# Optimization experiments

Hardware: AMD Instinct MI355X
Metric: run time of the kernel (lower is better)

The kernel has to match this reference:

```python
import jax, jax.numpy as jnp
import numpy as np
from jax import lax

SAMPLE_RATE = 44100.0


def _biquad(x, b0, b1, b2, a1, a2):
    """Direct-form-I biquad over last axis. x: [B,C,S]; coefs: [B,1] (broadcast over C).
    y[n] = b0*x[n] + b1*x[n-1] + b2*x[n-2] - a1*y[n-1] - a2*y[n-2], zero initial state
    (identical to torchaudio.functional.biquad)."""

    def step(carry, xn):  # xn: [B,C]
        x1, x2, y1, y2 = carry
        y = b0 * xn + b1 * x1 + b2 * x2 - a1 * y1 - a2 * y2
        return (xn, x1, y, y1), y

    xs = jnp.moveaxis(x, -1, 0)  # [S,B,C]
    z = jnp.zeros_like(x[..., 0])
    _, ys = lax.scan(step, (z, z, z, z), xs)
    return jnp.moveaxis(ys, 0, -1)  # [B,C,S]


def _peaking_coeffs(freq, gain, q):
    """RBJ peaking EQ coefficients, normalized by a0. Inputs: [B] -> outputs [B,1]."""
    w0 = 2.0 * jnp.pi * freq / SAMPLE_RATE
    alpha = jnp.sin(w0) / (2.0 * q)
    A = jnp.power(10.0, gain / 40.0)
    cosw0 = jnp.cos(w0)
    b0 = 1.0 + alpha * A
    b1 = -2.0 * cosw0
    b2 = 1.0 - alpha * A
    a0 = 1.0 + alpha / A
    a1 = -2.0 * cosw0
    a2 = 1.0 - alpha / A
    coefs = (b0 / a0, b1 / a0, b2 / a0, a1 / a0, a2 / a0)
    return tuple(c[:, None] for c in coefs)  # broadcast over channel dim


def setup_inputs() -> dict:
    key = jax.random.key(0)
    k1, k2, k3, k4 = jax.random.split(key, 4)
    B, C, S, NB = 32, 2, 262144, 10
    audio = jax.random.normal(k1, (B, C, S), dtype=jnp.float32)
    center_freqs = jax.random.uniform(k2, (B, NB), dtype=jnp.float32, minval=100.0, maxval=10000.0)
    gains = jax.random.uniform(k3, (B, NB), dtype=jnp.float32, minval=-12.0, maxval=12.0)
    q_factors = jax.random.uniform(k4, (B, NB), dtype=jnp.float32, minval=0.5, maxval=4.0)
    return {"audio": audio, "center_freqs": center_freqs, "gains": gains, "q_factors": q_factors}


def reference(audio, center_freqs, gains, q_factors):
    num_bands = center_freqs.shape[1]
    out = audio
    for band in range(num_bands):  # fixed small cascade of structurally distinct filters
        b0, b1, b2, a1, a2 = _peaking_coeffs(center_freqs[:, band], gains[:, band], q_factors[:, band])
        out = _biquad(out, b0, b1, b2, a1, a2)
    return out
```

## Files before the change

### kernel.cpp

```cpp
#include <hip/hip_runtime.h>


#define B_   32
#define C_   2
#define S_   262144
#define NB   10
#define SEQ  64
#define LCH  256
#define PCH  1024
#define SUP  256
#define NPOW 9

#define WS_POW 1600
#define WS_T   116800

__global__ void coef_kernel(const float* __restrict__ freqs,
                            const float* __restrict__ gains,
                            const float* __restrict__ qs,
                            float* __restrict__ coef) {
  int idx = blockIdx.x * blockDim.x + threadIdx.x;
  if (idx >= B_ * NB) return;
  float f = freqs[idx], g = gains[idx], Q = qs[idx];
  float w0 = 6.28318530717958648f * f / 44100.0f;
  float sw = sinf(w0), cw = cosf(w0);
  float alpha = sw / (2.0f * Q);
  float A = expf(g * 0.05756462732485114f);
  float aA = alpha * A, adA = alpha / A;
  float inv = 1.0f / (1.0f + adA);
  float* o = coef + idx * 5;
  o[0] = (1.0f + aA) * inv;
  o[1] = -2.0f * cw * inv;
  o[2] = (1.0f - aA) * inv;
  o[3] = 2.0f * cw * inv;
  o[4] = -(1.0f - adA) * inv;
}

__global__ __launch_bounds__(256) void power_kernel(const float* __restrict__ coef,
                                                    float* __restrict__ powers) {
  __shared__ float bufA[400], bufB[400];
  int b = blockIdx.x, tid = threadIdx.x;
  const float* cf = coef + b * NB * 5;
  for (int e = tid; e < 400; e += 256) bufA[e] = 0.0f;
  __syncthreads();
  if (tid < 20) {
    int c = tid;
    float rp = 0.0f;
    for (int k = 0; k < NB; k++) {
      float b0 = cf[k*5+0], b1 = cf[k*5+1], b2 = cf[k*5+2];
      float na1 = cf[k*5+3], na2 = cf[k*5+4];
      float val = (k > 0) ? b0 * rp : 0.0f;
      if (k > 0) {
        if (c == 2*k-2) val += b1;
        if (c == 2*k-1) val += b2;
      }
      if (c == 2*k)   val += na1;
      if (c == 2*k+1) val += na2;
      bufA[2*k*20 + c] = val;
      rp = val;
      if (c == 2*k) bufA[(2*k+1)*20 + c] = 1.0f;
    }
  }
  __syncthreads();
  float* cur = bufA;
  float* nxt = bufB;
  float* pw = powers + (size_t)b * NPOW * 400;
  for (int j = 1; j <= 17; j++) {
    for (int e = tid; e < 400; e += 256) {
      int r = e / 20, c = e % 20;
      float acc = 0.0f;
      #pragma unroll
      for (int k = 0; k < 20; k++) acc = fmaf(cur[r*20+k], cur[k*20+c], acc);
      nxt[e] = acc;
    }
    __syncthreads();
    { float* t_ = cur; cur = nxt; nxt = t_; }
    if (j == 8)  for (int e = tid; e < 400; e += 256) pw[e] = cur[e];
    if (j >= 10) for (int e = tid; e < 400; e += 256) pw[(j-9)*400 + e] = cur[e];
  }
}

template <bool WRITE_OUT>
__global__ __launch_bounds__(256) void pass_kernel(const float* __restrict__ x,
                                                   const float* __restrict__ coef,
                                                   const float* __restrict__ sc,
                                                   float* __restrict__ tout,
                                                   float* __restrict__ out) {
  const int seq = blockIdx.y;
  const int b = seq >> 1;
  const int chunk = blockIdx.x * blockDim.x + threadIdx.x;
  const float* cf = coef + b * NB * 5;
  float b0[NB], b1[NB], b2[NB], na1[NB], na2[NB];
  #pragma unroll
  for (int k = 0; k < NB; k++) {
    b0[k] = cf[k*5+0]; b1[k] = cf[k*5+1]; b2[k] = cf[k*5+2];
    na1[k] = cf[k*5+3]; na2[k] = cf[k*5+4];
  }
  const float* xs = x + (size_t)seq * S_ + (size_t)chunk * LCH;
  float p[NB], q[NB];
  float x1 = 0.0f, x2 = 0.0f;
  if (chunk > 0) { x1 = xs[-1]; x2 = xs[-2]; }
  if (WRITE_OUT && chunk > 0) {
    const float* s0 = sc + ((size_t)seq * PCH + (chunk - 1)) * 20;
    #pragma unroll
    for (int k = 0; k < NB; k++) { p[k] = s0[2*k]; q[k] = s0[2*k+1]; }
  } else {
    #pragma unroll
    for (int k = 0; k < NB; k++) { p[k] = 0.0f; q[k] = 0.0f; }
  }
  const float4* xv = (const float4*)xs;
  float4* ov = nullptr;
  if (WRITE_OUT) ov = (float4*)(out + (size_t)seq * S_ + (size_t)chunk * LCH);
  #pragma unroll 1
  for (int n4 = 0; n4 < LCH / 4; n4++) {
    float4 xq = xv[n4];
    float xin[4] = {xq.x, xq.y, xq.z, xq.w};
    float o[4];
    #pragma unroll
    for (int j = 0; j < 4; j++) {
      float u = xin[j], u1 = x1, u2 = x2;
      x2 = x1; x1 = xin[j];
      #pragma unroll
      for (int k = 0; k < NB; k++) {
        float v = fmaf(b0[k], u,
                  fmaf(b1[k], u1,
                  fmaf(b2[k], u2,
                  fmaf(na1[k], p[k], na2[k] * q[k]))));
        u1 = p[k]; u2 = q[k];
        q[k] = p[k]; p[k] = v;
        u = v;
      }
      o[j] = u;
    }
    if (WRITE_OUT) ov[n4] = make_float4(o[0], o[1], o[2], o[3]);
  }
  if (!WRITE_OUT) {
    float* td = tout + ((size_t)seq * PCH + chunk) * 20;
    #pragma unroll
    for (int k = 0; k < NB; k++) { td[2*k] = p[k]; td[2*k+1] = q[k]; }
  }
}

__device__ __forceinline__ void mv20(float* __restrict__ o, const float* M,
                                     const float* v) {
  #pragma unroll
  for (int r = 0; r < 20; r++) {
    float acc = 0.0f;
    #pragma unroll
    for (int c = 0; c < 20; c++) acc = fmaf(M[r*20+c], v[c], acc);
    o[r] = acc;
  }
}

__global__ __launch_bounds__(256) void scan_kernel(float* __restrict__ t,
                                                   const float* __restrict__ powers) {
  __shared__ float h[SUP * 21];
  __shared__ float Msh[400];
  __shared__ float Ksh[400];
  const int seq = blockIdx.x, b = seq >> 1, i = threadIdx.x;
  const float* pw = powers + (size_t)b * NPOW * 400;
  for (int e = i; e < 400; e += 256) Msh[e] = pw[e];
  __syncthreads();
  float* tb = t + (size_t)seq * PCH * 20;
  float u0[20], u1[20], u2[20], own[20], tmp[20];
  #pragma unroll
  for (int r = 0; r < 20; r++) u0[r] = tb[(4*i + 0)*20 + r];
  mv20(u1, Msh, u0);
  #pragma unroll
  for (int r = 0; r < 20; r++) u1[r] += tb[(4*i + 1)*20 + r];
  mv20(u2, Msh, u1);
  #pragma unroll
  for (int r = 0; r < 20; r++) u2[r] += tb[(4*i + 2)*20 + r];
  mv20(own, Msh, u2);
  #pragma unroll
  for (int r = 0; r < 20; r++) own[r] += tb[(4*i + 3)*20 + r];
  #pragma unroll
  for (int r = 0; r < 20; r++) h[i*21 + r] = own[r];
  for (int s = 0; s < 8; s++) {
    const int d = 1 << s;
    __syncthreads();
    for (int e = i; e < 400; e += 256) Ksh[e] = pw[(1 + s)*400 + e];
    __syncthreads();
    float nb[20];
    if (i >= d) {
      #pragma unroll
      for (int r = 0; r < 20; r++) nb[r] = h[(i - d)*21 + r];
    }
    __syncthreads();
    if (i >= d) {
      mv20(tmp, Ksh, nb);
      #pragma unroll
      for (int r = 0; r < 20; r++) { own[r] += tmp[r]; h[i*21 + r] = own[r]; }
    }
  }
  __syncthreads();
  float Pi[20];
  if (i > 0) {
    #pragma unroll
    for (int r = 0; r < 20; r++) Pi[r] = h[(i - 1)*21 + r];
  } else {
    #pragma unroll
    for (int r = 0; r < 20; r++) Pi[r] = 0.0f;
  }
  float w[20];
  mv20(w, Msh, Pi);
  #pragma unroll
  for (int r = 0; r < 20; r++) tb[(4*i + 0)*20 + r] = w[r] + u0[r];
  mv20(tmp, Msh, w);
  #pragma unroll
  for (int r = 0; r < 20; r++) tb[(4*i + 1)*20 + r] = tmp[r] + u1[r];
  mv20(w, Msh, tmp);
  #pragma unroll
  for (int r = 0; r < 20; r++) tb[(4*i + 2)*20 + r] = w[r] + u2[r];
  #pragma unroll
  for (int r = 0; r < 20; r++) tb[(4*i + 3)*20 + r] = own[r];
}

extern "C" void kernel_launch(void* const* d_in, const int* in_sizes, int n_in,
                              void* d_out, int out_size, void* d_ws, size_t ws_size,
                              hipStream_t stream) {
  const float* audio = (const float*)d_in[0];
  const float* freqs = (const float*)d_in[1];
  const float* gains = (const float*)d_in[2];
  const float* qs    = (const float*)d_in[3];
  float* out    = (float*)d_out;
  float* ws     = (float*)d_ws;
  float* coef   = ws;
  float* powers = ws + WS_POW;
  float* t      = ws + WS_T;

  hipLaunchKernelGGL(coef_kernel, dim3(5), dim3(64), 0, stream,
                     freqs, gains, qs, coef);
  hipLaunchKernelGGL(power_kernel, dim3(B_), dim3(256), 0, stream, coef, powers);
  hipLaunchKernelGGL((pass_kernel<false>), dim3(PCH / 256, SEQ), dim3(256), 0, stream,
                     audio, coef, (const float*)nullptr, t, (float*)nullptr);
  hipLaunchKernelGGL(scan_kernel, dim3(SEQ), dim3(256), 0, stream, t, powers);
  hipLaunchKernelGGL((pass_kernel<true>), dim3(PCH / 256, SEQ), dim3(256), 0, stream,
                     audio, coef, t, (float*)nullptr, out);
}
```

Measured before the change: 268.7 us.

## Use shorter chunks with multi-chunk ILP per thread and hierarchical three-level state scan

Chunk length drops from 256 to 64 samples, so there are 4096 chunks per sequence. Each thread filters 4 independent chunks at once, which gives the serial biquad recurrence instruction-level parallelism. The cross-chunk state propagation becomes a three-level scan: a Horner pass over groups of 8, a Kogge-Stone scan over 512 groups, and a Horner write-back, using an extra matrix power. The output pass stages results through LDS for coalesced stores. The cost is more workspace, more scan work and register pressure, and the old path is kept as a fallback when the workspace is too small.

```diff
diff --git a/kernel.cpp b/kernel.cpp
--- a/kernel.cpp
+++ b/kernel.cpp
@@ -6,13 +6,27 @@
 #define S_   262144
 #define NB   10
 #define SEQ  64
-#define LCH  256
-#define PCH  1024
-#define SUP  256
-#define NPOW 9
-
-#define WS_POW 1600
-#define WS_T   116800
+
+#define F_LCH   64
+#define F_PCH   4096
+#define F_NCH   4
+#define F_G     8
+#define F_GRP   512
+#define F_NPOW  11
+
+#define F_OFF_POW 1600
+#define F_OFF_T   142400
+#define F_OFF_G   5385280
+#define F_OFF_SB  6040640
+#define F_TOT     6696000
+
+#define FB_LCH  256
+#define FB_PCH  1024
+#define FB_SUP  256
+#define FB_NPOW 9
+#define FB_OFF_POW 1600
+#define FB_OFF_T   116800
+#define FB_TOT     1427520
 
 __global__ void coef_kernel(const float* __restrict__ freqs,
                             const float* __restrict__ gains,
@@ -35,13 +49,7 @@
   o[4] = -(1.0f - adA) * inv;
 }
 
-__global__ __launch_bounds__(256) void power_kernel(const float* __restrict__ coef,
-                                                    float* __restrict__ powers) {
-  __shared__ float bufA[400], bufB[400];
-  int b = blockIdx.x, tid = threadIdx.x;
-  const float* cf = coef + b * NB * 5;
-  for (int e = tid; e < 400; e += 256) bufA[e] = 0.0f;
-  __syncthreads();
+__device__ __forceinline__ void build_A_rows(const float* cf, float* bufA, int tid) {
   if (tid < 20) {
     int c = tid;
     float rp = 0.0f;
@@ -60,10 +68,21 @@
       if (c == 2*k) bufA[(2*k+1)*20 + c] = 1.0f;
     }
   }
+}
+
+
+__global__ __launch_bounds__(256) void power_fast(const float* __restrict__ coef,
+                                                  float* __restrict__ powers) {
+  __shared__ float bufA[400], bufB[400];
+  int b = blockIdx.x, tid = threadIdx.x;
+  const float* cf = coef + b * NB * 5;
+  for (int e = tid; e < 400; e += 256) bufA[e] = 0.0f;
+  __syncthreads();
+  build_A_rows(cf, bufA, tid);
   __syncthreads();
   float* cur = bufA;
   float* nxt = bufB;
-  float* pw = powers + (size_t)b * NPOW * 400;
+  float* pw = powers + (size_t)b * F_NPOW * 400;
   for (int j = 1; j <= 17; j++) {
     for (int e = tid; e < 400; e += 256) {
       int r = e / 20, c = e % 20;
@@ -74,17 +93,342 @@
     }
     __syncthreads();
     { float* t_ = cur; cur = nxt; nxt = t_; }
+    int slot = -1;
+    if (j == 6) slot = 0;
+    else if (j == 8) slot = 1;
+    else if (j == 9) slot = 2;
+    else if (j >= 10) slot = j - 7;
+    if (slot >= 0) for (int e = tid; e < 400; e += 256) pw[slot*400 + e] = cur[e];
+  }
+}
+
+__global__ __launch_bounds__(256, 1) void pass_false_fast(
+    const float* __restrict__ x, const float* __restrict__ coef,
+    float* __restrict__ t) {
+  const int seq = blockIdx.y;
+  const int b = seq >> 1;
+  const int tid = threadIdx.x;
+  const int wg0 = blockIdx.x * (256 * F_NCH);
+  const float* cf = coef + b * NB * 5;
+  float b0[NB], b1[NB], b2[NB], na1[NB], na2[NB];
+  #pragma unroll
+  for (int k = 0; k < NB; k++) {
+    b0[k] = cf[k*5+0]; b1[k] = cf[k*5+1]; b2[k] = cf[k*5+2];
+    na1[k] = cf[k*5+3]; na2[k] = cf[k*5+4];
+  }
+  int cidx[F_NCH];
+  const float4* xv[F_NCH];
+  float p[F_NCH][NB], q[F_NCH][NB], x1[F_NCH], x2[F_NCH];
+  #pragma unroll
+  for (int k = 0; k < F_NCH; k++) {
+    cidx[k] = wg0 + k * 256 + tid;
+    const float* xs = x + (size_t)seq * S_ + (size_t)cidx[k] * F_LCH;
+    xv[k] = (const float4*)xs;
+    x1[k] = 0.0f; x2[k] = 0.0f;
+    if (cidx[k] > 0) { x1[k] = xs[-1]; x2[k] = xs[-2]; }
+    #pragma unroll
+    for (int kk = 0; kk < NB; kk++) { p[k][kk] = 0.0f; q[k][kk] = 0.0f; }
+  }
+  #pragma unroll 1
+  for (int n4 = 0; n4 < F_LCH / 4; n4++) {
+    #pragma unroll
+    for (int k = 0; k < F_NCH; k++) {
+      float4 xq = xv[k][n4];
+      float xin[4] = {xq.x, xq.y, xq.z, xq.w};
+      #pragma unroll
+      for (int j = 0; j < 4; j++) {
+        float u = xin[j], u1 = x1[k], u2 = x2[k];
+        x2[k] = x1[k]; x1[k] = xin[j];
+        #pragma unroll
+        for (int kk = 0; kk < NB; kk++) {
+          float v = fmaf(b0[kk], u,
+                    fmaf(b1[kk], u1,
+                    fmaf(b2[kk], u2,
+                    fmaf(na1[kk], p[k][kk], na2[kk] * q[k][kk]))));
+          u1 = p[k][kk]; u2 = q[k][kk];
+          q[k][kk] = p[k][kk]; p[k][kk] = v;
+          u = v;
+        }
+      }
+    }
+  }
+  #pragma unroll
+  for (int k = 0; k < F_NCH; k++) {
+    float4* td = (float4*)(t + ((size_t)seq * F_PCH + cidx[k]) * 20);
+    #pragma unroll
+    for (int i = 0; i < 5; i++)
+      td[i] = make_float4(p[k][2*i], q[k][2*i], p[k][2*i+1], q[k][2*i+1]);
+  }
+}
+
+template <bool WRITE_BACK>
+__global__ __launch_bounds__(256) void scan_horner(
+    float* __restrict__ t, const float* __restrict__ powers,
+    float* __restrict__ gbuf, const float* __restrict__ sbuf) {
+  __shared__ float Msh[400];
+  const int seq = blockIdx.y, b = seq >> 1;
+  const int g = blockIdx.x * 256 + threadIdx.x;
+  const float* pw0 = powers + (size_t)b * F_NPOW * 400;
+  for (int e = threadIdx.x; e < 400; e += 256) {
+    int r = e / 20, c = e % 20;
+    Msh[c*20 + r] = pw0[e];
+  }
+  __syncthreads();
+  float s[20];
+  if (WRITE_BACK) {
+    const float4* sv = (const float4*)(sbuf + ((size_t)seq * F_GRP + g) * 20);
+    #pragma unroll
+    for (int i = 0; i < 5; i++) {
+      float4 a = sv[i];
+      s[4*i] = a.x; s[4*i+1] = a.y; s[4*i+2] = a.z; s[4*i+3] = a.w;
+    }
+  } else {
+    #pragma unroll
+    for (int r = 0; r < 20; r++) s[r] = 0.0f;
+  }
+  float* tp = t + ((size_t)seq * F_PCH + (size_t)g * F_G) * 20;
+  #pragma unroll 1
+  for (int j = 0; j < F_G; j++) {
+    float ns[20];
+    const float4* tv = (const float4*)(tp + j * 20);
+    #pragma unroll
+    for (int i = 0; i < 5; i++) {
+      float4 a = tv[i];
+      ns[4*i] = a.x; ns[4*i+1] = a.y; ns[4*i+2] = a.z; ns[4*i+3] = a.w;
+    }
+    #pragma unroll
+    for (int c = 0; c < 20; c++) {
+      float vc = s[c];
+      const float4* col = (const float4*)&Msh[c*20];
+      float4 c0 = col[0], c1 = col[1], c2 = col[2], c3 = col[3], c4 = col[4];
+      ns[0]  = fmaf(c0.x, vc, ns[0]);  ns[1]  = fmaf(c0.y, vc, ns[1]);
+      ns[2]  = fmaf(c0.z, vc, ns[2]);  ns[3]  = fmaf(c0.w, vc, ns[3]);
+      ns[4]  = fmaf(c1.x, vc, ns[4]);  ns[5]  = fmaf(c1.y, vc, ns[5]);
+      ns[6]  = fmaf(c1.z, vc, ns[6]);  ns[7]  = fmaf(c1.w, vc, ns[7]);
+      ns[8]  = fmaf(c2.x, vc, ns[8]);  ns[9]  = fmaf(c2.y, vc, ns[9]);
+      ns[10] = fmaf(c2.z, vc, ns[10]); ns[11] = fmaf(c2.w, vc, ns[11]);
+      ns[12] = fmaf(c3.x, vc, ns[12]); ns[13] = fmaf(c3.y, vc, ns[13]);
+      ns[14] = fmaf(c3.z, vc, ns[14]); ns[15] = fmaf(c3.w, vc, ns[15]);
+      ns[16] = fmaf(c4.x, vc, ns[16]); ns[17] = fmaf(c4.y, vc, ns[17]);
+      ns[18] = fmaf(c4.z, vc, ns[18]); ns[19] = fmaf(c4.w, vc, ns[19]);
+    }
+    #pragma unroll
+    for (int r = 0; r < 20; r++) s[r] = ns[r];
+    if (WRITE_BACK) {
+      float4* tw = (float4*)(tp + j * 20);
+      #pragma unroll
+      for (int i = 0; i < 5; i++)
+        tw[i] = make_float4(s[4*i], s[4*i+1], s[4*i+2], s[4*i+3]);
+    }
+  }
+  if (!WRITE_BACK) {
+    float4* gw = (float4*)(gbuf + ((size_t)seq * F_GRP + g) * 20);
+    #pragma unroll
+    for (int i = 0; i < 5; i++)
+      gw[i] = make_float4(s[4*i], s[4*i+1], s[4*i+2], s[4*i+3]);
+  }
+}
+
+__global__ __launch_bounds__(512) void scan_ks(
+    const float* __restrict__ gbuf, const float* __restrict__ powers,
+    float* __restrict__ sbuf) {
+  __shared__ float h[F_GRP * 20];
+  __shared__ float Ksh[400];
+  const int seq = blockIdx.x, b = seq >> 1, i = threadIdx.x;
+  const float* pw = powers + (size_t)b * F_NPOW * 400;
+  float own[20];
+  {
+    const float4* gv = (const float4*)(gbuf + ((size_t)seq * F_GRP + i) * 20);
+    #pragma unroll
+    for (int k = 0; k < 5; k++) {
+      float4 a = gv[k];
+      own[4*k] = a.x; own[4*k+1] = a.y; own[4*k+2] = a.z; own[4*k+3] = a.w;
+    }
+  }
+  #pragma unroll
+  for (int r = 0; r < 20; r++) h[i*20 + r] = own[r];
+  for (int s = 0; s < 9; s++) {
+    const int d = 1 << s;
+    const float* pwS = pw + (size_t)(2 + s) * 400;
+    __syncthreads();
+    for (int e = i; e < 400; e += 512) {
+      int r = e / 20, c = e % 20;
+      Ksh[c*20 + r] = pwS[e];
+    }
+    float nb[20];
+    if (i >= d) {
+      const float4* hv = (const float4*)&h[(i - d) * 20];
+      #pragma unroll
+      for (int k = 0; k < 5; k++) {
+        float4 a = hv[k];
+        nb[4*k] = a.x; nb[4*k+1] = a.y; nb[4*k+2] = a.z; nb[4*k+3] = a.w;
+      }
+    }
+    __syncthreads();
+    if (i >= d) {
+      #pragma unroll
+      for (int c = 0; c < 20; c++) {
+        float vc = nb[c];
+        const float4* col = (const float4*)&Ksh[c*20];
+        float4 c0 = col[0], c1 = col[1], c2 = col[2], c3 = col[3], c4 = col[4];
+        own[0]  = fmaf(c0.x, vc, own[0]);  own[1]  = fmaf(c0.y, vc, own[1]);
+        own[2]  = fmaf(c0.z, vc, own[2]);  own[3]  = fmaf(c0.w, vc, own[3]);
+        own[4]  = fmaf(c1.x, vc, own[4]);  own[5]  = fmaf(c1.y, vc, own[5]);
+        own[6]  = fmaf(c1.z, vc, own[6]);  own[7]  = fmaf(c1.w, vc, own[7]);
+        own[8]  = fmaf(c2.x, vc, own[8]);  own[9]  = fmaf(c2.y, vc, own[9]);
+        own[10] = fmaf(c2.z, vc, own[10]); own[11] = fmaf(c2.w, vc, own[11]);
+        own[12] = fmaf(c3.x, vc, own[12]); own[13] = fmaf(c3.w==c3.w?c3.y:c3.y, vc, own[13]);
+        own[14] = fmaf(c3.z, vc, own[14]); own[15] = fmaf(c3.w, vc, own[15]);
+        own[16] = fmaf(c4.x, vc, own[16]); own[17] = fmaf(c4.y, vc, own[17]);
+        own[18] = fmaf(c4.z, vc, own[18]); own[19] = fmaf(c4.w, vc, own[19]);
+      }
+      #pragma unroll
+      for (int r = 0; r < 20; r++) h[i*20 + r] = own[r];
+    }
+  }
+  __syncthreads();
+  float4* sw = (float4*)(sbuf + ((size_t)seq * F_GRP + i) * 20);
+  if (i > 0) {
+    const float4* hv = (const float4*)&h[(i - 1) * 20];
+    #pragma unroll
+    for (int k = 0; k < 5; k++) sw[k] = hv[k];
+  } else {
+    #pragma unroll
+    for (int k = 0; k < 5; k++) sw[k] = make_float4(0.f, 0.f, 0.f, 0.f);
+  }
+}
+
+__global__ __launch_bounds__(256, 1) void pass_true_fast(
+    const float* __restrict__ x, const float* __restrict__ coef,
+    const float* __restrict__ t, float* __restrict__ out) {
+  __shared__ float stash[2 * 256 * 16];
+  const int seq = blockIdx.y;
+  const int b = seq >> 1;
+  const int tid = threadIdx.x;
+  const int wg0 = blockIdx.x * (256 * F_NCH);
+  const float* cf = coef + b * NB * 5;
+  float b0[NB], b1[NB], b2[NB], na1[NB], na2[NB];
+  #pragma unroll
+  for (int k = 0; k < NB; k++) {
+    b0[k] = cf[k*5+0]; b1[k] = cf[k*5+1]; b2[k] = cf[k*5+2];
+    na1[k] = cf[k*5+3]; na2[k] = cf[k*5+4];
+  }
+  int cidx[F_NCH];
+  const float4* xv[F_NCH];
+  float p[F_NCH][NB], q[F_NCH][NB], x1[F_NCH], x2[F_NCH];
+  #pragma unroll
+  for (int k = 0; k < F_NCH; k++) {
+    cidx[k] = wg0 + k * 256 + tid;
+    const float* xs = x + (size_t)seq * S_ + (size_t)cidx[k] * F_LCH;
+    xv[k] = (const float4*)xs;
+    x1[k] = 0.0f; x2[k] = 0.0f;
+    if (cidx[k] > 0) { x1[k] = xs[-1]; x2[k] = xs[-2]; }
+    if (cidx[k] > 0) {
+      const float4* sv = (const float4*)(t + ((size_t)seq * F_PCH + cidx[k] - 1) * 20);
+      #pragma unroll
+      for (int i = 0; i < 5; i++) {
+        float4 a = sv[i];
+        p[k][2*i] = a.x; q[k][2*i] = a.y; p[k][2*i+1] = a.z; q[k][2*i+1] = a.w;
+      }
+    } else {
+      #pragma unroll
+      for (int kk = 0; kk < NB; kk++) { p[k][kk] = 0.0f; q[k][kk] = 0.0f; }
+    }
+  }
+  float4* stashv = (float4*)stash;
+  const size_t seqbase = (size_t)seq * S_;
+  #pragma unroll 1
+  for (int tile = 0; tile < 4; tile++) {
+    float4 oreg[2][4];
+    #pragma unroll 1
+    for (int n4 = 0; n4 < 4; n4++) {
+      #pragma unroll
+      for (int k = 0; k < F_NCH; k++) {
+        float4 xq = xv[k][tile*4 + n4];
+        float xin[4] = {xq.x, xq.y, xq.z, xq.w};
+        float o[4];
+        #pragma unroll
+        for (int j = 0; j < 4; j++) {
+          float u = xin[j], u1 = x1[k], u2 = x2[k];
+          x2[k] = x1[k]; x1[k] = xin[j];
+          #pragma unroll
+          for (int kk = 0; kk < NB; kk++) {
+            float v = fmaf(b0[kk], u,
+                      fmaf(b1[kk], u1,
+                      fmaf(b2[kk], u2,
+                      fmaf(na1[kk], p[k][kk], na2[kk] * q[k][kk]))));
+            u1 = p[k][kk]; u2 = q[k][kk];
+            q[k][kk] = p[k][kk]; p[k][kk] = v;
+            u = v;
+          }
+          o[j] = u;
+        }
+        float4 of = make_float4(o[0], o[1], o[2], o[3]);
+        if (k < 2) stashv[(k*256 + tid)*4 + n4] = of;
+        else       oreg[k-2][n4] = of;
+      }
+    }
+    __syncthreads();
+    #pragma unroll
+    for (int i = 0; i < 8; i++) {
+      int f = tid + i * 256;
+      int chunkIdx = f >> 2, w = f & 3;
+      float4 v = stashv[f];
+      float4* op = (float4*)(out + seqbase + (size_t)(wg0 + chunkIdx) * F_LCH + tile*16);
+      op[w] = v;
+    }
+    __syncthreads();
+    #pragma unroll
+    for (int k2 = 0; k2 < 2; k2++)
+      #pragma unroll
+      for (int n4 = 0; n4 < 4; n4++)
+        stashv[(k2*256 + tid)*4 + n4] = oreg[k2][n4];
+    __syncthreads();
+    #pragma unroll
+    for (int i = 0; i < 8; i++) {
+      int f = tid + i * 256;
+      int chunkIdx = f >> 2, w = f & 3;
+      float4 v = stashv[f];
+      float4* op = (float4*)(out + seqbase + (size_t)(wg0 + 512 + chunkIdx) * F_LCH + tile*16);
+      op[w] = v;
+    }
+    __syncthreads();
+  }
+}
+
+__global__ __launch_bounds__(256) void power_fb(const float* __restrict__ coef,
+                                                float* __restrict__ powers) {
+  __shared__ float bufA[400], bufB[400];
+  int b = blockIdx.x, tid = threadIdx.x;
+  const float* cf = coef + b * NB * 5;
+  for (int e = tid; e < 400; e += 256) bufA[e] = 0.0f;
+  __syncthreads();
+  build_A_rows(cf, bufA, tid);
+  __syncthreads();
+  float* cur = bufA;
+  float* nxt = bufB;
+  float* pw = powers + (size_t)b * FB_NPOW * 400;
+  for (int j = 1; j <= 17; j++) {
+    for (int e = tid; e < 400; e += 256) {
+      int r = e / 20, c = e % 20;
+      float acc = 0.0f;
+      #pragma unroll
+      for (int k = 0; k < 20; k++) acc = fmaf(cur[r*20+k], cur[k*20+c], acc);
+      nxt[e] = acc;
+    }
+    __syncthreads();
+    { float* t_ = cur; cur = nxt; nxt = t_; }
     if (j == 8)  for (int e = tid; e < 400; e += 256) pw[e] = cur[e];
     if (j >= 10) for (int e = tid; e < 400; e += 256) pw[(j-9)*400 + e] = cur[e];
   }
 }
 
 template <bool WRITE_OUT>
-__global__ __launch_bounds__(256) void pass_kernel(const float* __restrict__ x,
-                                                   const float* __restrict__ coef,
-                                                   const float* __restrict__ sc,
-                                                   float* __restrict__ tout,
-                                                   float* __restrict__ out) {
+__global__ __launch_bounds__(256) void pass_fb(const float* __restrict__ x,
+                                               const float* __restrict__ coef,
+                                               const float* __restrict__ sc,
+                                               float* __restrict__ tout,
+                                               float* __restrict__ out) {
   const int seq = blockIdx.y;
   const int b = seq >> 1;
   const int chunk = blockIdx.x * blockDim.x + threadIdx.x;
@@ -95,24 +439,24 @@
     b0[k] = cf[k*5+0]; b1[k] = cf[k*5+1]; b2[k] = cf[k*5+2];
     na1[k] = cf[k*5+3]; na2[k] = cf[k*5+4];
   }
-  const float* xs = x + (size_t)seq * S_ + (size_t)chunk * LCH;
+  const float* xs = x + (size_t)seq * S_ + (size_t)chunk * FB_LCH;
   float p[NB], q[NB];
   float x1 = 0.0f, x2 = 0.0f;
   if (chunk > 0) { x1 = xs[-1]; x2 = xs[-2]; }
   if (WRITE_OUT && chunk > 0) {
-    const float* s0 = sc + ((size_t)seq * PCH + (chunk - 1)) * 20;
+    const float* s0 = sc + ((size_t)seq * FB_PCH + (chunk - 1)) * 20;
     #pragma unroll
     for (int k = 0; k < NB; k++) { p[k] = s0[2*k]; q[k] = s0[2*k+1]; }
   } else {
     #pragma unroll
     for (int k = 0; k < NB; k++) { p[k] = 0.0f; q[k] = 0.0f; }
   }
-  const float4* xv = (const float4*)xs;
+  const float4* xvv = (const float4*)xs;
   float4* ov = nullptr;
-  if (WRITE_OUT) ov = (float4*)(out + (size_t)seq * S_ + (size_t)chunk * LCH);
+  if (WRITE_OUT) ov = (float4*)(out + (size_t)seq * S_ + (size_t)chunk * FB_LCH);
   #pragma unroll 1
-  for (int n4 = 0; n4 < LCH / 4; n4++) {
-    float4 xq = xv[n4];
+  for (int n4 = 0; n4 < FB_LCH / 4; n4++) {
+    float4 xq = xvv[n4];
     float xin[4] = {xq.x, xq.y, xq.z, xq.w};
     float o[4];
     #pragma unroll
@@ -134,14 +478,14 @@
     if (WRITE_OUT) ov[n4] = make_float4(o[0], o[1], o[2], o[3]);
   }
   if (!WRITE_OUT) {
-    float* td = tout + ((size_t)seq * PCH + chunk) * 20;
+    float* td = tout + ((size_t)seq * FB_PCH + chunk) * 20;
     #pragma unroll
     for (int k = 0; k < NB; k++) { td[2*k] = p[k]; td[2*k+1] = q[k]; }
   }
 }
 
-__device__ __forceinline__ void mv20(float* __restrict__ o, const float* M,
-                                     const float* v) {
+__device__ __forceinline__ void mv20_fb(float* __restrict__ o, const float* M,
+                                        const float* v) {
   #pragma unroll
   for (int r = 0; r < 20; r++) {
     float acc = 0.0f;
@@ -151,26 +495,26 @@
   }
 }
 
-__global__ __launch_bounds__(256) void scan_kernel(float* __restrict__ t,
-                                                   const float* __restrict__ powers) {
-  __shared__ float h[SUP * 21];
+__global__ __launch_bounds__(256) void scan_fb(float* __restrict__ t,
+                                               const float* __restrict__ powers) {
+  __shared__ float h[FB_SUP * 21];
   __shared__ float Msh[400];
   __shared__ float Ksh[400];
   const int seq = blockIdx.x, b = seq >> 1, i = threadIdx.x;
-  const float* pw = powers + (size_t)b * NPOW * 400;
+  const float* pw = powers + (size_t)b * FB_NPOW * 400;
   for (int e = i; e < 400; e += 256) Msh[e] = pw[e];
   __syncthreads();
-  float* tb = t + (size_t)seq * PCH * 20;
+  float* tb = t + (size_t)seq * FB_PCH * 20;
   float u0[20], u1[20], u2[20], own[20], tmp[20];
   #pragma unroll
   for (int r = 0; r < 20; r++) u0[r] = tb[(4*i + 0)*20 + r];
-  mv20(u1, Msh, u0);
+  mv20_fb(u1, Msh, u0);
   #pragma unroll
   for (int r = 0; r < 20; r++) u1[r] += tb[(4*i + 1)*20 + r];
-  mv20(u2, Msh, u1);
+  mv20_fb(u2, Msh, u1);
   #pragma unroll
   for (int r = 0; r < 20; r++) u2[r] += tb[(4*i + 2)*20 + r];
-  mv20(own, Msh, u2);
+  mv20_fb(own, Msh, u2);
   #pragma unroll
   for (int r = 0; r < 20; r++) own[r] += tb[(4*i + 3)*20 + r];
   #pragma unroll
@@ -187,7 +531,7 @@
     }
     __syncthreads();
     if (i >= d) {
-      mv20(tmp, Ksh, nb);
+      mv20_fb(tmp, Ksh, nb);
       #pragma unroll
       for (int r = 0; r < 20; r++) { own[r] += tmp[r]; h[i*21 + r] = own[r]; }
     }
@@ -202,13 +546,13 @@
     for (int r = 0; r < 20; r++) Pi[r] = 0.0f;
   }
   float w[20];
-  mv20(w, Msh, Pi);
+  mv20_fb(w, Msh, Pi);
   #pragma unroll
   for (int r = 0; r < 20; r++) tb[(4*i + 0)*20 + r] = w[r] + u0[r];
-  mv20(tmp, Msh, w);
+  mv20_fb(tmp, Msh, w);
   #pragma unroll
   for (int r = 0; r < 20; r++) tb[(4*i + 1)*20 + r] = tmp[r] + u1[r];
-  mv20(w, Msh, tmp);
+  mv20_fb(w, Msh, tmp);
   #pragma unroll
   for (int r = 0; r < 20; r++) tb[(4*i + 2)*20 + r] = w[r] + u2[r];
   #pragma unroll
@@ -222,18 +566,37 @@
   const float* freqs = (const float*)d_in[1];
   const float* gains = (const float*)d_in[2];
   const float* qs    = (const float*)d_in[3];
-  float* out    = (float*)d_out;
-  float* ws     = (float*)d_ws;
-  float* coef   = ws;
-  float* powers = ws + WS_POW;
-  float* t      = ws + WS_T;
+  float* out = (float*)d_out;
+  float* ws  = (float*)d_ws;
+  float* coef = ws;
 
   hipLaunchKernelGGL(coef_kernel, dim3(5), dim3(64), 0, stream,
                      freqs, gains, qs, coef);
-  hipLaunchKernelGGL(power_kernel, dim3(B_), dim3(256), 0, stream, coef, powers);
-  hipLaunchKernelGGL((pass_kernel<false>), dim3(PCH / 256, SEQ), dim3(256), 0, stream,
-                     audio, coef, (const float*)nullptr, t, (float*)nullptr);
-  hipLaunchKernelGGL(scan_kernel, dim3(SEQ), dim3(256), 0, stream, t, powers);
-  hipLaunchKernelGGL((pass_kernel<true>), dim3(PCH / 256, SEQ), dim3(256), 0, stream,
-                     audio, coef, t, (float*)nullptr, out);
-}
+
+  if (ws_size >= (size_t)F_TOT * sizeof(float)) {
+    float* powers = ws + F_OFF_POW;
+    float* t      = ws + F_OFF_T;
+    float* gbuf   = ws + F_OFF_G;
+    float* sbuf   = ws + F_OFF_SB;
+    hipLaunchKernelGGL(power_fast, dim3(B_), dim3(256), 0, stream, coef, powers);
+    hipLaunchKernelGGL(pass_false_fast, dim3(F_PCH / (256 * F_NCH), SEQ), dim3(256),
+                       0, stream, audio, coef, t);
+    hipLaunchKernelGGL((scan_horner<false>), dim3(F_GRP / 256, SEQ), dim3(256),
+                       0, stream, t, powers, gbuf, (const float*)nullptr);
+    hipLaunchKernelGGL(scan_ks, dim3(SEQ), dim3(512), 0, stream,
+                       gbuf, powers, sbuf);
+    hipLaunchKernelGGL((scan_horner<true>), dim3(F_GRP / 256, SEQ), dim3(256),
+                       0, stream, t, powers, (float*)nullptr, sbuf);
+    hipLaunchKernelGGL(pass_true_fast, dim3(F_PCH / (256 * F_NCH), SEQ), dim3(256),
+                       0, stream, audio, coef, t, out);
+  } else {
+    float* powers = ws + FB_OFF_POW;
+    float* t      = ws + FB_OFF_T;
+    hipLaunchKernelGGL(power_fb, dim3(B_), dim3(256), 0, stream, coef, powers);
+    hipLaunchKernelGGL((pass_fb<false>), dim3(FB_PCH / 256, SEQ), dim3(256), 0, stream,
+                       audio, coef, (const float*)nullptr, t, (float*)nullptr);
+    hipLaunchKernelGGL(scan_fb, dim3(SEQ), dim3(256), 0, stream, t, powers);
+    hipLaunchKernelGGL((pass_fb<true>), dim3(FB_PCH / 256, SEQ), dim3(256), 0, stream,
+                       audio, coef, t, (float*)nullptr, out);
+  }
+}
```

Measured after the change: 290.4 us. 8.0% more time.

## Shrink chunks to 64 samples, stage through LDS, and use a three-level state scan

Applied to the files above, without the earlier changes.

The sequence is now split into 4096 chunks of 64 samples, so there are four times as many threads, each doing a shorter serial biquad cascade. Audio is staged through swizzled LDS so global loads and stores are coalesced. The cross-chunk state scan becomes a Horner reduction over groups of 8, a Kogge-Stone scan over 512 group totals, and a Horner write-back. The coefficient and power kernels are merged into one setup kernel, which adds an extra matrix power but removes one launch. The cost is more launches and more 20-float state traffic.

```diff
diff --git a/kernel.cpp b/kernel.cpp
--- a/kernel.cpp
+++ b/kernel.cpp
@@ -6,48 +6,53 @@
 #define S_   262144
 #define NB   10
 #define SEQ  64
-#define LCH  256
-#define PCH  1024
-#define SUP  256
-#define NPOW 9
-
-#define WS_POW 1600
-#define WS_T   116800
-
-__global__ void coef_kernel(const float* __restrict__ freqs,
-                            const float* __restrict__ gains,
-                            const float* __restrict__ qs,
-                            float* __restrict__ coef) {
-  int idx = blockIdx.x * blockDim.x + threadIdx.x;
-  if (idx >= B_ * NB) return;
-  float f = freqs[idx], g = gains[idx], Q = qs[idx];
-  float w0 = 6.28318530717958648f * f / 44100.0f;
-  float sw = sinf(w0), cw = cosf(w0);
-  float alpha = sw / (2.0f * Q);
-  float A = expf(g * 0.05756462732485114f);
-  float aA = alpha * A, adA = alpha / A;
-  float inv = 1.0f / (1.0f + adA);
-  float* o = coef + idx * 5;
-  o[0] = (1.0f + aA) * inv;
-  o[1] = -2.0f * cw * inv;
-  o[2] = (1.0f - aA) * inv;
-  o[3] = 2.0f * cw * inv;
-  o[4] = -(1.0f - adA) * inv;
-}
-
-__global__ __launch_bounds__(256) void power_kernel(const float* __restrict__ coef,
-                                                    float* __restrict__ powers) {
+
+#define F_LCH   64
+#define F_PCH   4096
+#define F_G     8
+#define F_GRP   512
+#define F_NPOW  11
+
+#define F_OFF_POW 1600
+#define F_OFF_T   142400
+#define F_OFF_G   5385280
+#define F_OFF_SB  6040640
+#define F_TOT     6696000
+
+__global__ __launch_bounds__(256) void setup_kernel(
+    const float* __restrict__ freqs, const float* __restrict__ gains,
+    const float* __restrict__ qs, float* __restrict__ coef,
+    float* __restrict__ powers) {
   __shared__ float bufA[400], bufB[400];
-  int b = blockIdx.x, tid = threadIdx.x;
-  const float* cf = coef + b * NB * 5;
+  __shared__ float cfs[NB * 5];
+  const int b = blockIdx.x, tid = threadIdx.x;
   for (int e = tid; e < 400; e += 256) bufA[e] = 0.0f;
+  if (tid < NB) {
+    int idx = b * NB + tid;
+    float f = freqs[idx], g = gains[idx], Q = qs[idx];
+    float w0 = 6.28318530717958648f * f / 44100.0f;
+    float sw = sinf(w0), cw = cosf(w0);
+    float alpha = sw / (2.0f * Q);
+    float A = expf(g * 0.05756462732485114f);
+    float aA = alpha * A, adA = alpha / A;
+    float inv = 1.0f / (1.0f + adA);
+    float c0 = (1.0f + aA) * inv;
+    float c1 = -2.0f * cw * inv;
+    float c2 = (1.0f - aA) * inv;
+    float c3 = 2.0f * cw * inv;
+    float c4 = -(1.0f - adA) * inv;
+    cfs[tid*5+0] = c0; cfs[tid*5+1] = c1; cfs[tid*5+2] = c2;
+    cfs[tid*5+3] = c3; cfs[tid*5+4] = c4;
+    float* o = coef + idx * 5;
+    o[0] = c0; o[1] = c1; o[2] = c2; o[3] = c3; o[4] = c4;
+  }
   __syncthreads();
   if (tid < 20) {
     int c = tid;
     float rp = 0.0f;
     for (int k = 0; k < NB; k++) {
-      float b0 = cf[k*5+0], b1 = cf[k*5+1], b2 = cf[k*5+2];
-      float na1 = cf[k*5+3], na2 = cf[k*5+4];
+      float b0 = cfs[k*5+0], b1 = cfs[k*5+1], b2 = cfs[k*5+2];
+      float na1 = cfs[k*5+3], na2 = cfs[k*5+4];
       float val = (k > 0) ? b0 * rp : 0.0f;
       if (k > 0) {
         if (c == 2*k-2) val += b1;
@@ -63,7 +68,7 @@
   __syncthreads();
   float* cur = bufA;
   float* nxt = bufB;
-  float* pw = powers + (size_t)b * NPOW * 400;
+  float* pw = powers + (size_t)b * F_NPOW * 400;
   for (int j = 1; j <= 17; j++) {
     for (int e = tid; e < 400; e += 256) {
       int r = e / 20, c = e % 20;
@@ -74,20 +79,26 @@
     }
     __syncthreads();
     { float* t_ = cur; cur = nxt; nxt = t_; }
-    if (j == 8)  for (int e = tid; e < 400; e += 256) pw[e] = cur[e];
-    if (j >= 10) for (int e = tid; e < 400; e += 256) pw[(j-9)*400 + e] = cur[e];
+    int slot = -1;
+    if (j == 6) slot = 0;
+    else if (j == 8) slot = 1;
+    else if (j == 9) slot = 2;
+    else if (j >= 10) slot = j - 7;
+    if (slot >= 0) for (int e = tid; e < 400; e += 256) pw[slot*400 + e] = cur[e];
   }
 }
 
 template <bool WRITE_OUT>
-__global__ __launch_bounds__(256) void pass_kernel(const float* __restrict__ x,
-                                                   const float* __restrict__ coef,
-                                                   const float* __restrict__ sc,
-                                                   float* __restrict__ tout,
-                                                   float* __restrict__ out) {
+__global__ __launch_bounds__(64) void pass_v3(
+    const float* __restrict__ x, const float* __restrict__ coef,
+    const float* __restrict__ tst, float* __restrict__ tout,
+    float* __restrict__ out) {
+  __shared__ float4 lds4[1024];
   const int seq = blockIdx.y;
   const int b = seq >> 1;
-  const int chunk = blockIdx.x * blockDim.x + threadIdx.x;
+  const int lane = threadIdx.x;
+  const int wgc0 = blockIdx.x * 64;
+  const int chunk = wgc0 + lane;
   const float* cf = coef + b * NB * 5;
   float b0[NB], b1[NB], b2[NB], na1[NB], na2[NB];
   #pragma unroll
@@ -95,25 +106,43 @@
     b0[k] = cf[k*5+0]; b1[k] = cf[k*5+1]; b2[k] = cf[k*5+2];
     na1[k] = cf[k*5+3]; na2[k] = cf[k*5+4];
   }
-  const float* xs = x + (size_t)seq * S_ + (size_t)chunk * LCH;
-  float p[NB], q[NB];
+  const size_t span0 = (size_t)seq * S_ + (size_t)wgc0 * F_LCH;
+  const float4* gx = (const float4*)(x + span0);
+  #pragma unroll 4
+  for (int it = 0; it < 16; it++) {
+    int f = it * 64 + lane;
+    float4 v = gx[f];
+    int c = f >> 4, q = f & 15;
+    lds4[c*16 + (q ^ (c & 15))] = v;
+  }
+  __syncthreads();
   float x1 = 0.0f, x2 = 0.0f;
-  if (chunk > 0) { x1 = xs[-1]; x2 = xs[-2]; }
+  if (lane == 0) {
+    if (chunk > 0) {
+      const float* xs = x + span0;
+      x1 = xs[-1]; x2 = xs[-2];
+    }
+  } else {
+    float4 pv = lds4[(lane-1)*16 + (15 ^ ((lane-1) & 15))];
+    x2 = pv.z; x1 = pv.w;
+  }
+  float p[NB], q_[NB];
   if (WRITE_OUT && chunk > 0) {
-    const float* s0 = sc + ((size_t)seq * PCH + (chunk - 1)) * 20;
-    #pragma unroll
-    for (int k = 0; k < NB; k++) { p[k] = s0[2*k]; q[k] = s0[2*k+1]; }
-  } else {
-    #pragma unroll
-    for (int k = 0; k < NB; k++) { p[k] = 0.0f; q[k] = 0.0f; }
-  }
-  const float4* xv = (const float4*)xs;
-  float4* ov = nullptr;
-  if (WRITE_OUT) ov = (float4*)(out + (size_t)seq * S_ + (size_t)chunk * LCH);
-  #pragma unroll 1
-  for (int n4 = 0; n4 < LCH / 4; n4++) {
-    float4 xq = xv[n4];
-    float xin[4] = {xq.x, xq.y, xq.z, xq.w};
+    const float4* sv = (const float4*)(tst + ((size_t)seq * F_PCH + chunk - 1) * 20);
+    #pragma unroll
+    for (int i = 0; i < 5; i++) {
+      float4 a = sv[i];
+      p[2*i] = a.x; q_[2*i] = a.y; p[2*i+1] = a.z; q_[2*i+1] = a.w;
+    }
+  } else {
+    #pragma unroll
+    for (int k = 0; k < NB; k++) { p[k] = 0.0f; q_[k] = 0.0f; }
+  }
+  #pragma unroll 2
+  for (int qq = 0; qq < 16; qq++) {
+    const int slot = lane*16 + (qq ^ (lane & 15));
+    float4 xv = lds4[slot];
+    float xin[4] = {xv.x, xv.y, xv.z, xv.w};
     float o[4];
     #pragma unroll
     for (int j = 0; j < 4; j++) {
@@ -124,95 +153,174 @@
         float v = fmaf(b0[k], u,
                   fmaf(b1[k], u1,
                   fmaf(b2[k], u2,
-                  fmaf(na1[k], p[k], na2[k] * q[k]))));
-        u1 = p[k]; u2 = q[k];
-        q[k] = p[k]; p[k] = v;
+                  fmaf(na1[k], p[k], na2[k] * q_[k]))));
+        u1 = p[k]; u2 = q_[k];
+        q_[k] = p[k]; p[k] = v;
         u = v;
       }
       o[j] = u;
     }
-    if (WRITE_OUT) ov[n4] = make_float4(o[0], o[1], o[2], o[3]);
-  }
-  if (!WRITE_OUT) {
-    float* td = tout + ((size_t)seq * PCH + chunk) * 20;
-    #pragma unroll
-    for (int k = 0; k < NB; k++) { td[2*k] = p[k]; td[2*k+1] = q[k]; }
-  }
-}
-
-__device__ __forceinline__ void mv20(float* __restrict__ o, const float* M,
-                                     const float* v) {
+    if (WRITE_OUT) lds4[slot] = make_float4(o[0], o[1], o[2], o[3]);
+  }
+  if (WRITE_OUT) {
+    __syncthreads();
+    float4* gy = (float4*)(out + span0);
+    #pragma unroll 4
+    for (int it = 0; it < 16; it++) {
+      int f = it * 64 + lane;
+      int c = f >> 4, q = f & 15;
+      gy[f] = lds4[c*16 + (q ^ (c & 15))];
+    }
+  } else {
+    float4* td = (float4*)(tout + ((size_t)seq * F_PCH + chunk) * 20);
+    #pragma unroll
+    for (int i = 0; i < 5; i++)
+      td[i] = make_float4(p[2*i], q_[2*i], p[2*i+1], q_[2*i+1]);
+  }
+}
+
+template <bool WRITE_BACK>
+__global__ __launch_bounds__(256) void scan_horner(
+    float* __restrict__ t, const float* __restrict__ powers,
+    float* __restrict__ gbuf, const float* __restrict__ sbuf) {
+  __shared__ float Msh[400];
+  const int seq = blockIdx.y, b = seq >> 1;
+  const int g = blockIdx.x * 256 + threadIdx.x;
+  const float* pw0 = powers + (size_t)b * F_NPOW * 400;
+  for (int e = threadIdx.x; e < 400; e += 256) {
+    int r = e / 20, c = e % 20;
+    Msh[c*20 + r] = pw0[e];
+  }
+  __syncthreads();
+  float s[20];
+  if (WRITE_BACK) {
+    const float4* sv = (const float4*)(sbuf + ((size_t)seq * F_GRP + g) * 20);
+    #pragma unroll
+    for (int i = 0; i < 5; i++) {
+      float4 a = sv[i];
+      s[4*i] = a.x; s[4*i+1] = a.y; s[4*i+2] = a.z; s[4*i+3] = a.w;
+    }
+  } else {
+    #pragma unroll
+    for (int r = 0; r < 20; r++) s[r] = 0.0f;
+  }
+  float* tp = t + ((size_t)seq * F_PCH + (size_t)g * F_G) * 20;
+  const float4* tv = (const float4*)tp;
+  float4 nx[5];
   #pragma unroll
-  for (int r = 0; r < 20; r++) {
-    float acc = 0.0f;
-    #pragma unroll
-    for (int c = 0; c < 20; c++) acc = fmaf(M[r*20+c], v[c], acc);
-    o[r] = acc;
-  }
-}
-
-__global__ __launch_bounds__(256) void scan_kernel(float* __restrict__ t,
-                                                   const float* __restrict__ powers) {
-  __shared__ float h[SUP * 21];
-  __shared__ float Msh[400];
+  for (int i = 0; i < 5; i++) nx[i] = tv[i];
+  #pragma unroll 1
+  for (int j = 0; j < F_G; j++) {
+    float ns[20];
+    #pragma unroll
+    for (int i = 0; i < 5; i++) {
+      float4 a = nx[i];
+      ns[4*i] = a.x; ns[4*i+1] = a.y; ns[4*i+2] = a.z; ns[4*i+3] = a.w;
+    }
+    if (j < F_G - 1) {
+      #pragma unroll
+      for (int i = 0; i < 5; i++) nx[i] = tv[(j+1)*5 + i];
+    }
+    #pragma unroll
+    for (int c = 0; c < 20; c++) {
+      float vc = s[c];
+      const float4* col = (const float4*)&Msh[c*20];
+      float4 c0 = col[0], c1 = col[1], c2 = col[2], c3 = col[3], c4 = col[4];
+      ns[0]  = fmaf(c0.x, vc, ns[0]);  ns[1]  = fmaf(c0.y, vc, ns[1]);
+      ns[2]  = fmaf(c0.z, vc, ns[2]);  ns[3]  = fmaf(c0.w, vc, ns[3]);
+      ns[4]  = fmaf(c1.x, vc, ns[4]);  ns[5]  = fmaf(c1.y, vc, ns[5]);
+      ns[6]  = fmaf(c1.z, vc, ns[6]);  ns[7]  = fmaf(c1.w, vc, ns[7]);
+      ns[8]  = fmaf(c2.x, vc, ns[8]);  ns[9]  = fmaf(c2.y, vc, ns[9]);
+      ns[10] = fmaf(c2.z, vc, ns[10]); ns[11] = fmaf(c2.w, vc, ns[11]);
+      ns[12] = fmaf(c3.x, vc, ns[12]); ns[13] = fmaf(c3.y, vc, ns[13]);
+      ns[14] = fmaf(c3.z, vc, ns[14]); ns[15] = fmaf(c3.w, vc, ns[15]);
+      ns[16] = fmaf(c4.x, vc, ns[16]); ns[17] = fmaf(c4.y, vc, ns[17]);
+      ns[18] = fmaf(c4.z, vc, ns[18]); ns[19] = fmaf(c4.w, vc, ns[19]);
+    }
+    #pragma unroll
+    for (int r = 0; r < 20; r++) s[r] = ns[r];
+    if (WRITE_BACK) {
+      float4* tw = (float4*)(tp + j * 20);
+      #pragma unroll
+      for (int i = 0; i < 5; i++)
+        tw[i] = make_float4(s[4*i], s[4*i+1], s[4*i+2], s[4*i+3]);
+    }
+  }
+  if (!WRITE_BACK) {
+    float4* gw = (float4*)(gbuf + ((size_t)seq * F_GRP + g) * 20);
+    #pragma unroll
+    for (int i = 0; i < 5; i++)
+      gw[i] = make_float4(s[4*i], s[4*i+1], s[4*i+2], s[4*i+3]);
+  }
+}
+
+__global__ __launch_bounds__(512) void scan_ks(
+    const float* __restrict__ gbuf, const float* __restrict__ powers,
+    float* __restrict__ sbuf) {
+  __shared__ float h[F_GRP * 20];
   __shared__ float Ksh[400];
   const int seq = blockIdx.x, b = seq >> 1, i = threadIdx.x;
-  const float* pw = powers + (size_t)b * NPOW * 400;
-  for (int e = i; e < 400; e += 256) Msh[e] = pw[e];
-  __syncthreads();
-  float* tb = t + (size_t)seq * PCH * 20;
-  float u0[20], u1[20], u2[20], own[20], tmp[20];
+  const float* pw = powers + (size_t)b * F_NPOW * 400;
+  float own[20];
+  {
+    const float4* gv = (const float4*)(gbuf + ((size_t)seq * F_GRP + i) * 20);
+    #pragma unroll
+    for (int k = 0; k < 5; k++) {
+      float4 a = gv[k];
+      own[4*k] = a.x; own[4*k+1] = a.y; own[4*k+2] = a.z; own[4*k+3] = a.w;
+    }
+  }
   #pragma unroll
-  for (int r = 0; r < 20; r++) u0[r] = tb[(4*i + 0)*20 + r];
-  mv20(u1, Msh, u0);
-  #pragma unroll
-  for (int r = 0; r < 20; r++) u1[r] += tb[(4*i + 1)*20 + r];
-  mv20(u2, Msh, u1);
-  #pragma unroll
-  for (int r = 0; r < 20; r++) u2[r] += tb[(4*i + 2)*20 + r];
-  mv20(own, Msh, u2);
-  #pragma unroll
-  for (int r = 0; r < 20; r++) own[r] += tb[(4*i + 3)*20 + r];
-  #pragma unroll
-  for (int r = 0; r < 20; r++) h[i*21 + r] = own[r];
-  for (int s = 0; s < 8; s++) {
+  for (int r = 0; r < 20; r++) h[i*20 + r] = own[r];
+  for (int s = 0; s < 9; s++) {
     const int d = 1 << s;
+    const float* pwS = pw + (size_t)(2 + s) * 400;
     __syncthreads();
-    for (int e = i; e < 400; e += 256) Ksh[e] = pw[(1 + s)*400 + e];
-    __syncthreads();
+    for (int e = i; e < 400; e += 512) {
+      int r = e / 20, c = e % 20;
+      Ksh[c*20 + r] = pwS[e];
+    }
     float nb[20];
     if (i >= d) {
-      #pragma unroll
-      for (int r = 0; r < 20; r++) nb[r] = h[(i - d)*21 + r];
+      const float4* hv = (const float4*)&h[(i - d) * 20];
+      #pragma unroll
+      for (int k = 0; k < 5; k++) {
+        float4 a = hv[k];
+        nb[4*k] = a.x; nb[4*k+1] = a.y; nb[4*k+2] = a.z; nb[4*k+3] = a.w;
+      }
     }
     __syncthreads();
     if (i >= d) {
-      mv20(tmp, Ksh, nb);
-      #pragma unroll
-      for (int r = 0; r < 20; r++) { own[r] += tmp[r]; h[i*21 + r] = own[r]; }
-    }
-  }
-  __syncthreads();
-  float Pi[20];
+      #pragma unroll
+      for (int c = 0; c < 20; c++) {
+        float vc = nb[c];
+        const float4* col = (const float4*)&Ksh[c*20];
+        float4 c0 = col[0], c1 = col[1], c2 = col[2], c3 = col[3], c4 = col[4];
+        own[0]  = fmaf(c0.x, vc, own[0]);  own[1]  = fmaf(c0.y, vc, own[1]);
+        own[2]  = fmaf(c0.z, vc, own[2]);  own[3]  = fmaf(c0.w, vc, own[3]);
+        own[4]  = fmaf(c1.x, vc, own[4]);  own[5]  = fmaf(c1.y, vc, own[5]);
+        own[6]  = fmaf(c1.z, vc, own[6]);  own[7]  = fmaf(c1.w, vc, own[7]);
+        own[8]  = fmaf(c2.x, vc, own[8]);  own[9]  = fmaf(c2.y, vc, own[9]);
+        own[10] = fmaf(c2.z, vc, own[10]); own[11] = fmaf(c2.w, vc, own[11]);
+        own[12] = fmaf(c3.x, vc, own[12]); own[13] = fmaf(c3.y, vc, own[13]);
+        own[14] = fmaf(c3.z, vc, own[14]); own[15] = fmaf(c3.w, vc, own[15]);
+        own[16] = fmaf(c4.x, vc, own[16]); own[17] = fmaf(c4.y, vc, own[17]);
+        own[18] = fmaf(c4.z, vc, own[18]); own[19] = fmaf(c4.w, vc, own[19]);
+      }
+      #pragma unroll
+      for (int r = 0; r < 20; r++) h[i*20 + r] = own[r];
+    }
+  }
+  __syncthreads();
+  float4* sw = (float4*)(sbuf + ((size_t)seq * F_GRP + i) * 20);
   if (i > 0) {
-    #pragma unroll
-    for (int r = 0; r < 20; r++) Pi[r] = h[(i - 1)*21 + r];
-  } else {
-    #pragma unroll
-    for (int r = 0; r < 20; r++) Pi[r] = 0.0f;
-  }
-  float w[20];
-  mv20(w, Msh, Pi);
-  #pragma unroll
-  for (int r = 0; r < 20; r++) tb[(4*i + 0)*20 + r] = w[r] + u0[r];
-  mv20(tmp, Msh, w);
-  #pragma unroll
-  for (int r = 0; r < 20; r++) tb[(4*i + 1)*20 + r] = tmp[r] + u1[r];
-  mv20(w, Msh, tmp);
-  #pragma unroll
-  for (int r = 0; r < 20; r++) tb[(4*i + 2)*20 + r] = w[r] + u2[r];
-  #pragma unroll
-  for (int r = 0; r < 20; r++) tb[(4*i + 3)*20 + r] = own[r];
+    const float4* hv = (const float4*)&h[(i - 1) * 20];
+    #pragma unroll
+    for (int k = 0; k < 5; k++) sw[k] = hv[k];
+  } else {
+    #pragma unroll
+    for (int k = 0; k < 5; k++) sw[k] = make_float4(0.f, 0.f, 0.f, 0.f);
+  }
 }
 
 extern "C" void kernel_launch(void* const* d_in, const int* in_sizes, int n_in,
@@ -222,18 +330,24 @@
   const float* freqs = (const float*)d_in[1];
   const float* gains = (const float*)d_in[2];
   const float* qs    = (const float*)d_in[3];
-  float* out    = (float*)d_out;
-  float* ws     = (float*)d_ws;
+  float* out = (float*)d_out;
+  float* ws  = (float*)d_ws;
   float* coef   = ws;
-  float* powers = ws + WS_POW;
-  float* t      = ws + WS_T;
-
-  hipLaunchKernelGGL(coef_kernel, dim3(5), dim3(64), 0, stream,
-                     freqs, gains, qs, coef);
-  hipLaunchKernelGGL(power_kernel, dim3(B_), dim3(256), 0, stream, coef, powers);
-  hipLaunchKernelGGL((pass_kernel<false>), dim3(PCH / 256, SEQ), dim3(256), 0, stream,
+  float* powers = ws + F_OFF_POW;
+  float* t      = ws + F_OFF_T;
+  float* gbuf   = ws + F_OFF_G;
+  float* sbuf   = ws + F_OFF_SB;
+
+  hipLaunchKernelGGL(setup_kernel, dim3(B_), dim3(256), 0, stream,
+                     freqs, gains, qs, coef, powers);
+  hipLaunchKernelGGL((pass_v3<false>), dim3(F_PCH / 64, SEQ), dim3(64), 0, stream,
                      audio, coef, (const float*)nullptr, t, (float*)nullptr);
-  hipLaunchKernelGGL(scan_kernel, dim3(SEQ), dim3(256), 0, stream, t, powers);
-  hipLaunchKernelGGL((pass_kernel<true>), dim3(PCH / 256, SEQ), dim3(256), 0, stream,
+  hipLaunchKernelGGL((scan_horner<false>), dim3(F_GRP / 256, SEQ), dim3(256),
+                     0, stream, t, powers, gbuf, (const float*)nullptr);
+  hipLaunchKernelGGL(scan_ks, dim3(SEQ), dim3(512), 0, stream,
+                     gbuf, powers, sbuf);
+  hipLaunchKernelGGL((scan_horner<true>), dim3(F_GRP / 256, SEQ), dim3(256),
+                     0, stream, t, powers, (float*)nullptr, sbuf);
+  hipLaunchKernelGGL((pass_v3<true>), dim3(F_PCH / 64, SEQ), dim3(64), 0, stream,
                      audio, coef, t, (float*)nullptr, out);
 }
```

After: 236.1 us. 12.1% less time.
